# Kernel tuning notes

Measured on AMD Instinct MI355X. Metric: run time of the kernel, lower is better.

Reference implementation:

```python
import jax, jax.numpy as jnp
import numpy as np


def setup_inputs() -> dict:
    key = jax.random.key(0)
    ks = jax.random.split(key, 5)
    B, S, H = 4, 4096, 512
    std = 1.0 / np.sqrt(H)
    x = jax.random.normal(ks[0], (B, S, H), dtype=jnp.float32)
    relative_pos = jax.random.normal(ks[1], (B, S, H), dtype=jnp.float32)
    Wq = jax.random.normal(ks[2], (H, H), dtype=jnp.float32) * std
    Wk = jax.random.normal(ks[3], (H, H), dtype=jnp.float32) * std
    Wv = jax.random.normal(ks[4], (H, H), dtype=jnp.float32) * std
    bq = jnp.zeros((H,), dtype=jnp.float32)
    bk = jnp.zeros((H,), dtype=jnp.float32)
    bv = jnp.zeros((H,), dtype=jnp.float32)
    return {"x": x, "relative_pos": relative_pos, "Wq": Wq, "bq": bq,
            "Wk": Wk, "bk": bk, "Wv": Wv, "bv": bv}


def reference(x, relative_pos, Wq, bq, Wk, bk, Wv, bv):
    H = x.shape[-1]
    scale = jnp.sqrt(jnp.asarray(H, dtype=x.dtype))
    # torch Linear: y = x @ W^T + b
    Q = jnp.einsum('bsh,oh->bso', x, Wq) + bq
    K = jnp.einsum('bsh,oh->bso', x, Wk) + bk
    V = jnp.einsum('bsh,oh->bso', x, Wv) + bv
    Kr = jnp.einsum('bsh,oh->bso', relative_pos, Wk) + bk
    # two score terms, each [B,S,S]
    scores = (jnp.einsum('bqd,bkd->bqk', Q, K) +
              jnp.einsum('bqd,bkd->bqk', Q, Kr)) / scale
    weights = jax.nn.softmax(scores, axis=-1)
    return jnp.einsum('bqk,bkd->bqd', weights, V)
```

## Files before the change

### kernel.cpp

```cpp
#include <hip/hip_runtime.h>
#include <stdint.h>

typedef __attribute__((ext_vector_type(8))) short bf16x8;
typedef __attribute__((ext_vector_type(4))) float f32x4;

#define AS1 __attribute__((address_space(1)))
#define AS3 __attribute__((address_space(3)))

__device__ __forceinline__ void gl2lds16(const void* g, void* l) {
    __builtin_amdgcn_global_load_lds((const AS1 void*)g, (AS3 void*)l, 16, 0, 0);
}

__device__ __forceinline__ unsigned short f2bf(float f) {
    uint32_t u = __builtin_bit_cast(uint32_t, f);
    uint32_t r = (u + 0x7fffu + ((u >> 16) & 1u)) >> 16;
    return (unsigned short)r;
}

constexpr int S = 4096;
constexpr int H = 512;
constexpr size_t OFF_XB  = 0;
constexpr size_t OFF_SB  = 16777216;
constexpr size_t OFF_WQB = 33554432;
constexpr size_t OFF_WKB = 34078720;
constexpr size_t OFF_WVB = 34603008;
constexpr size_t OFF_BQK = 35127296;
constexpr size_t OFF_QB  = 35131392;
constexpr size_t OFF_K2B = OFF_QB  + 16777216;
constexpr size_t OFF_VTB = OFF_K2B + 16777216;
constexpr size_t OFF_PB  = OFF_VTB + 16777216;
constexpr size_t OFF_L   = OFF_PB  + 134217728;

__global__ __launch_bounds__(256) void prep_all(const float* __restrict__ x,
                                                const float* __restrict__ rp,
                                                const float* __restrict__ wq,
                                                const float* __restrict__ wk,
                                                const float* __restrict__ wv,
                                                const float* __restrict__ bq,
                                                const float* __restrict__ bk,
                                                unsigned short* __restrict__ xb,
                                                unsigned short* __restrict__ sb,
                                                unsigned short* __restrict__ wqb,
                                                unsigned short* __restrict__ wkb,
                                                unsigned short* __restrict__ wvb,
                                                float* __restrict__ bqk,
                                                float* __restrict__ lrow) {
    if (blockIdx.x < 8192) {
        const int i = (blockIdx.x * 256 + threadIdx.x) * 4;
        float4 xv = *(const float4*)(x + i);
        float4 rv = *(const float4*)(rp + i);
        uint2 xo, so;
        xo.x = (uint32_t)f2bf(xv.x) | ((uint32_t)f2bf(xv.y) << 16);
        xo.y = (uint32_t)f2bf(xv.z) | ((uint32_t)f2bf(xv.w) << 16);
        so.x = (uint32_t)f2bf(xv.x + rv.x) | ((uint32_t)f2bf(xv.y + rv.y) << 16);
        so.y = (uint32_t)f2bf(xv.z + rv.z) | ((uint32_t)f2bf(xv.w + rv.w) << 16);
        *(uint2*)(xb + i) = xo;
        *(uint2*)(sb + i) = so;
    } else {
        const int t = (blockIdx.x - 8192) * 256 + threadIdx.x;
        const int i = t * 4;
        float4 q = *(const float4*)(wq + i);
        float4 k = *(const float4*)(wk + i);
        float4 v = *(const float4*)(wv + i);
        uint2 o;
        o.x = (uint32_t)f2bf(q.x) | ((uint32_t)f2bf(q.y) << 16);
        o.y = (uint32_t)f2bf(q.z) | ((uint32_t)f2bf(q.w) << 16);
        *(uint2*)(wqb + i) = o;
        o.x = (uint32_t)f2bf(k.x) | ((uint32_t)f2bf(k.y) << 16);
        o.y = (uint32_t)f2bf(k.z) | ((uint32_t)f2bf(k.w) << 16);
        *(uint2*)(wkb + i) = o;
        o.x = (uint32_t)f2bf(v.x) | ((uint32_t)f2bf(v.y) << 16);
        o.y = (uint32_t)f2bf(v.z) | ((uint32_t)f2bf(v.w) << 16);
        *(uint2*)(wvb + i) = o;
        if (t < 128) {
            *(float4*)(bqk + t * 4) = *(const float4*)(bq + t * 4);
        } else if (t < 256) {
            const int u = t - 128;
            float4 b = *(const float4*)(bk + u * 4);
            *(float4*)(bqk + 512 + u * 4) = make_float4(2.f * b.x, 2.f * b.y, 2.f * b.z, 2.f * b.w);
        }
        if (t < 4096) {
            *(float4*)(lrow + t * 4) = make_float4(0.f, 0.f, 0.f, 0.f);
        }
    }
}

template <int MODE, int SWZ, int NP64>
__global__ __launch_bounds__(256, 2)
void gemm_bt(const unsigned short* __restrict__ Abase,
             const unsigned short* __restrict__ Bbase,
             void* __restrict__ Cbase,
             int M, int N, int K,
             long long sAz, long long sBz, long long sCz,
             const float* __restrict__ bias_n, long long sBNz,
             const float* __restrict__ bias_m,
             float scale,
             float* __restrict__ rowdiv, long long sRz)
{
    int bx = blockIdx.x, by = blockIdx.y, bz = blockIdx.z;
    if (SWZ) {
        const int gx = gridDim.x, gy = gridDim.y;
        const int id  = bx + gx * (by + gridDim.y * bz);
        const int xcd = id & 7;
        const int k   = id >> 3;
        const int kg  = k / gx;
        bx = k - kg * gx;
        const int g = xcd + 8 * kg;
        const int gz = g / gy;
        by = g - gz * gy;
        bz = gz;
    }
    const int z = bz;
    const unsigned short* A  = Abase + (size_t)z * (size_t)sAz;
    const unsigned short* Bm = Bbase + (size_t)z * (size_t)sBz;
    const int bn = bx * 128;
    const int bm = by * 128;

    constexpr int STAGE_BYTES = NP64 * 32768;
    constexpr int SMEM_BYTES = (MODE == 1) ? STAGE_BYTES
                             : (STAGE_BYTES > 34816 ? STAGE_BYTES : 34816);
    __shared__ __align__(16) char smem[SMEM_BYTES];
    char* As = smem;
    char* Bs = smem + NP64 * 16384;

    const int tid  = threadIdx.x;
    const int wave = tid >> 6;
    const int lane = tid & 63;
    const int lm   = lane & 15;
    const int quad = lane >> 4;
    const int wm   = (wave >> 1) * 64;
    const int wn   = (wave & 1) * 64;

    const int sr = wave * 8 + (lane >> 3);
    const int ss = ((lane & 7) ^ (lane >> 3)) * 8;

    const int sA0 = (quad ^ (lm & 7)) * 16;

    f32x4 acc[4][4] = {};

    for (int k0 = 0; k0 < K; k0 += 64 * NP64) {
        __syncthreads();
        #pragma unroll
        for (int pp = 0; pp < NP64; pp++) {
            const unsigned short* Ap = A  + (size_t)(bm + sr) * K + k0 + pp * 64 + ss;
            const unsigned short* Bp = Bm + (size_t)(bn + sr) * K + k0 + pp * 64 + ss;
            char* Asp = As + pp * 16384 + wave * 1024;
            char* Bsp = Bs + pp * 16384 + wave * 1024;
            #pragma unroll
            for (int c = 0; c < 4; c++) {
                gl2lds16(Ap + (size_t)(c * 32) * K, Asp + c * 4096);
                gl2lds16(Bp + (size_t)(c * 32) * K, Bsp + c * 4096);
            }
        }
        __syncthreads();

        #pragma unroll
        for (int pp = 0; pp < NP64; pp++) {
            #pragma unroll
            for (int ks = 0; ks < 2; ks++) {
                const int so = ks ? (sA0 ^ 64) : sA0;
                bf16x8 af[4], bfr[4];
                #pragma unroll
                for (int t = 0; t < 4; t++)
                    af[t]  = *(const bf16x8*)(As + pp * 16384 + (wm + t * 16 + lm) * 128 + so);
                #pragma unroll
                for (int t = 0; t < 4; t++)
                    bfr[t] = *(const bf16x8*)(Bs + pp * 16384 + (wn + t * 16 + lm) * 128 + so);
                #pragma unroll
                for (int mt = 0; mt < 4; mt++)
                    #pragma unroll
                    for (int nt = 0; nt < 4; nt++)
                        acc[mt][nt] = __builtin_amdgcn_mfma_f32_16x16x32_bf16(af[mt], bfr[nt], acc[mt][nt], 0, 0, 0);
            }
        }
    }

    if (MODE == 1) {
        float* C = (float*)Cbase + (size_t)z * (size_t)sCz;
        const float* rd = rowdiv + (size_t)z * (size_t)sRz;
        #pragma unroll
        for (int mt = 0; mt < 4; mt++) {
            #pragma unroll
            for (int i = 0; i < 4; i++) {
                const int row = bm + wm + mt * 16 + quad * 4 + i;
                const float inv = 1.0f / rd[row];
                const size_t rb = (size_t)row * (size_t)N;
                #pragma unroll
                for (int nt = 0; nt < 4; nt++) {
                    const int col = bn + wn + nt * 16 + lm;
                    C[rb + col] = acc[mt][nt][i] * inv;
                }
            }
        }
    } else {
        unsigned short* C = (unsigned short*)Cbase + (size_t)z * (size_t)sCz;
        const float* bn_ptr = (MODE == 0 && bias_n) ? bias_n + (size_t)z * (size_t)sBNz : nullptr;
        float* lr = (MODE == 2) ? rowdiv + (size_t)z * (size_t)sRz : nullptr;
        unsigned short* Ct = (unsigned short*)smem;
        __syncthreads();
        #pragma unroll
        for (int mt = 0; mt < 4; mt++) {
            #pragma unroll
            for (int i = 0; i < 4; i++) {
                const int r = wm + mt * 16 + quad * 4 + i;
                if (MODE == 0) {
                    const float badd = bias_m ? bias_m[bm + r] : 0.0f;
                    #pragma unroll
                    for (int nt = 0; nt < 4; nt++) {
                        const int col = bn + wn + nt * 16 + lm;
                        float v = acc[mt][nt][i] * scale + badd;
                        if (bn_ptr) v += bn_ptr[col];
                        Ct[r * 136 + wn + nt * 16 + lm] = f2bf(v);
                    }
                } else {
                    float rsum = 0.f;
                    #pragma unroll
                    for (int nt = 0; nt < 4; nt++) {
                        float p = __expf(acc[mt][nt][i] * scale);
                        rsum += p;
                        Ct[r * 136 + wn + nt * 16 + lm] = f2bf(p);
                    }
                    rsum += __shfl_xor(rsum, 1);
                    rsum += __shfl_xor(rsum, 2);
                    rsum += __shfl_xor(rsum, 4);
                    rsum += __shfl_xor(rsum, 8);
                    if (lm == 0) atomicAdd(lr + bm + r, rsum);
                }
            }
        }
        __syncthreads();
        #pragma unroll
        for (int j = 0; j < 8; j++) {
            const int r   = (tid >> 4) + 16 * j;
            const int c16 = tid & 15;
            uint4 vv = *(const uint4*)(Ct + r * 136 + c16 * 8);
            *(uint4*)(C + (size_t)(bm + r) * (size_t)N + bn + c16 * 8) = vv;
        }
    }
}

extern "C" void kernel_launch(void* const* d_in, const int* in_sizes, int n_in,
                              void* d_out, int out_size, void* d_ws, size_t ws_size,
                              hipStream_t stream) {
    const float* x  = (const float*)d_in[0];
    const float* rp = (const float*)d_in[1];
    const float* Wq = (const float*)d_in[2];
    const float* bq = (const float*)d_in[3];
    const float* Wk = (const float*)d_in[4];
    const float* bk = (const float*)d_in[5];
    const float* Wv = (const float*)d_in[6];
    const float* bv = (const float*)d_in[7];

    char* ws = (char*)d_ws;
    unsigned short* xb  = (unsigned short*)(ws + OFF_XB);
    unsigned short* sb  = (unsigned short*)(ws + OFF_SB);
    unsigned short* wqb = (unsigned short*)(ws + OFF_WQB);
    unsigned short* wkb = (unsigned short*)(ws + OFF_WKB);
    unsigned short* wvb = (unsigned short*)(ws + OFF_WVB);
    float*          bqk = (float*)(ws + OFF_BQK);
    unsigned short* qb  = (unsigned short*)(ws + OFF_QB);
    unsigned short* k2b = (unsigned short*)(ws + OFF_K2B);
    unsigned short* vtb = (unsigned short*)(ws + OFF_VTB);
    unsigned short* pb  = (unsigned short*)(ws + OFF_PB);
    float*          lrow = (float*)(ws + OFF_L);

    prep_all<<<8448, 256, 0, stream>>>(x, rp, Wq, Wk, Wv, bq, bk,
                                       xb, sb, wqb, wkb, wvb, bqk, lrow);

    gemm_bt<0, 1, 1><<<dim3(4, 128, 2), 256, 0, stream>>>(
        xb, wqb, qb, 16384, 512, 512,
        8388608, 262144, 8388608,
        bqk, 512, nullptr, 1.0f, nullptr, 0);
    gemm_bt<0, 0, 1><<<dim3(32, 4, 4), 256, 0, stream>>>(
        wvb, xb, vtb, 512, 4096, 512,
        0, (long long)S * H, (long long)S * H,
        nullptr, 0, bv, 1.0f, nullptr, 0);
    gemm_bt<2, 0, 1><<<dim3(32, 32, 4), 256, 0, stream>>>(
        qb, k2b, pb, 4096, 4096, 512,
        (long long)S * H, (long long)S * H, (long long)S * S,
        nullptr, 0, nullptr, 0.044194173824159216f,
        lrow, 4096);
    gemm_bt<1, 1, 2><<<dim3(4, 32, 4), 256, 0, stream>>>(
        pb, vtb, d_out, 4096, 512, 4096,
        (long long)S * S, (long long)S * H, (long long)S * H,
        nullptr, 0, nullptr, 1.0f, lrow, 4096);
}
```

Baseline: 331.8 us.

## Add dedicated 128x256-tile score kernel with fused exp and row-sum epilogue

Replaces the generic MODE 2 GEMM for the QK^T score stage with a specialized kernel. It uses 512 threads and a 128x256 output tile, so each loaded B tile is reused across more rows and fewer blocks are launched. The kernel keeps the fused exp, row-sum atomic and bf16 store epilogue, writing in two 128-column halves through LDS. The larger tile raises register and LDS use per block, which may reduce occupancy. The MODE 2 path in the generic kernel is removed.

```diff
diff --git a/kernel.cpp b/kernel.cpp
--- a/kernel.cpp
+++ b/kernel.cpp
@@ -133,7 +133,6 @@
 
     const int sr = wave * 8 + (lane >> 3);
     const int ss = ((lane & 7) ^ (lane >> 3)) * 8;
-
     const int sA0 = (quad ^ (lm & 7)) * 16;
 
     f32x4 acc[4][4] = {};
@@ -194,8 +193,7 @@
         }
     } else {
         unsigned short* C = (unsigned short*)Cbase + (size_t)z * (size_t)sCz;
-        const float* bn_ptr = (MODE == 0 && bias_n) ? bias_n + (size_t)z * (size_t)sBNz : nullptr;
-        float* lr = (MODE == 2) ? rowdiv + (size_t)z * (size_t)sRz : nullptr;
+        const float* bn_ptr = bias_n ? bias_n + (size_t)z * (size_t)sBNz : nullptr;
         unsigned short* Ct = (unsigned short*)smem;
         __syncthreads();
         #pragma unroll
@@ -203,22 +201,110 @@
             #pragma unroll
             for (int i = 0; i < 4; i++) {
                 const int r = wm + mt * 16 + quad * 4 + i;
-                if (MODE == 0) {
-                    const float badd = bias_m ? bias_m[bm + r] : 0.0f;
-                    #pragma unroll
-                    for (int nt = 0; nt < 4; nt++) {
-                        const int col = bn + wn + nt * 16 + lm;
-                        float v = acc[mt][nt][i] * scale + badd;
-                        if (bn_ptr) v += bn_ptr[col];
-                        Ct[r * 136 + wn + nt * 16 + lm] = f2bf(v);
-                    }
-                } else {
+                const float badd = bias_m ? bias_m[bm + r] : 0.0f;
+                #pragma unroll
+                for (int nt = 0; nt < 4; nt++) {
+                    const int col = bn + wn + nt * 16 + lm;
+                    float v = acc[mt][nt][i] * scale + badd;
+                    if (bn_ptr) v += bn_ptr[col];
+                    Ct[r * 136 + wn + nt * 16 + lm] = f2bf(v);
+                }
+            }
+        }
+        __syncthreads();
+        #pragma unroll
+        for (int j = 0; j < 8; j++) {
+            const int r   = (tid >> 4) + 16 * j;
+            const int c16 = tid & 15;
+            uint4 vv = *(const uint4*)(Ct + r * 136 + c16 * 8);
+            *(uint4*)(C + (size_t)(bm + r) * (size_t)N + bn + c16 * 8) = vv;
+        }
+    }
+}
+
+__global__ __launch_bounds__(512, 4)
+void score_bt(const unsigned short* __restrict__ Qb,
+              const unsigned short* __restrict__ K2b,
+              unsigned short* __restrict__ Pb,
+              float* __restrict__ lrow)
+{
+    constexpr int N  = 4096;
+    constexpr int Kd = 512;
+    constexpr float scale = 0.044194173824159216f;
+    __shared__ __align__(16) char smem[49152];
+    char* As = smem;
+    char* Bs = smem + 16384;
+
+    const int bx = blockIdx.x, by = blockIdx.y, z = blockIdx.z;
+    const int bn = bx * 256;
+    const int bm = by * 128;
+    const unsigned short* Az = Qb  + (size_t)z * (size_t)N * Kd;
+    const unsigned short* Bz = K2b + (size_t)z * (size_t)N * Kd;
+
+    const int tid  = threadIdx.x;
+    const int wave = tid >> 6;
+    const int lane = tid & 63;
+    const int lm   = lane & 15;
+    const int quad = lane >> 4;
+    const int wm   = (wave >> 2) * 64;
+    const int wn   = (wave & 3) * 64;
+
+    const int sr = wave * 8 + (lane >> 3);
+    const int ss = ((lane & 7) ^ (lane >> 3)) * 8;
+    const int sA0 = (quad ^ (lm & 7)) * 16;
+
+    f32x4 acc[4][4] = {};
+
+    for (int k0 = 0; k0 < Kd; k0 += 64) {
+        __syncthreads();
+        const unsigned short* Ap = Az + (size_t)(bm + sr) * Kd + k0 + ss;
+        const unsigned short* Bp = Bz + (size_t)(bn + sr) * Kd + k0 + ss;
+        char* Asp = As + wave * 1024;
+        char* Bsp = Bs + wave * 1024;
+        gl2lds16(Ap,                   Asp);
+        gl2lds16(Ap + (size_t)64 * Kd, Asp + 8192);
+        #pragma unroll
+        for (int c = 0; c < 4; c++)
+            gl2lds16(Bp + (size_t)(c * 64) * Kd, Bsp + c * 8192);
+        __syncthreads();
+
+        #pragma unroll
+        for (int ks = 0; ks < 2; ks++) {
+            const int so = ks ? (sA0 ^ 64) : sA0;
+            bf16x8 af[4], bfr[4];
+            #pragma unroll
+            for (int t = 0; t < 4; t++)
+                af[t]  = *(const bf16x8*)(As + (wm + t * 16 + lm) * 128 + so);
+            #pragma unroll
+            for (int t = 0; t < 4; t++)
+                bfr[t] = *(const bf16x8*)(Bs + (wn + t * 16 + lm) * 128 + so);
+            #pragma unroll
+            for (int mt = 0; mt < 4; mt++)
+                #pragma unroll
+                for (int nt = 0; nt < 4; nt++)
+                    acc[mt][nt] = __builtin_amdgcn_mfma_f32_16x16x32_bf16(af[mt], bfr[nt], acc[mt][nt], 0, 0, 0);
+        }
+    }
+
+    __syncthreads();
+    unsigned short* Ct = (unsigned short*)smem;
+    float* lr = lrow + (size_t)z * 4096;
+    unsigned short* Cz = Pb + (size_t)z * (size_t)N * N;
+
+    #pragma unroll
+    for (int nh = 0; nh < 2; ++nh) {
+        if ((wn >> 7) == nh) {
+            #pragma unroll
+            for (int mt = 0; mt < 4; mt++) {
+                #pragma unroll
+                for (int i = 0; i < 4; i++) {
+                    const int r = wm + mt * 16 + quad * 4 + i;
                     float rsum = 0.f;
                     #pragma unroll
                     for (int nt = 0; nt < 4; nt++) {
                         float p = __expf(acc[mt][nt][i] * scale);
                         rsum += p;
-                        Ct[r * 136 + wn + nt * 16 + lm] = f2bf(p);
+                        Ct[r * 136 + (wn & 64) + nt * 16 + lm] = f2bf(p);
                     }
                     rsum += __shfl_xor(rsum, 1);
                     rsum += __shfl_xor(rsum, 2);
@@ -230,12 +316,13 @@
         }
         __syncthreads();
         #pragma unroll
-        for (int j = 0; j < 8; j++) {
-            const int r   = (tid >> 4) + 16 * j;
+        for (int j = 0; j < 4; j++) {
+            const int r   = (tid >> 4) + 32 * j;
             const int c16 = tid & 15;
             uint4 vv = *(const uint4*)(Ct + r * 136 + c16 * 8);
-            *(uint4*)(C + (size_t)(bm + r) * (size_t)N + bn + c16 * 8) = vv;
-        }
+            *(uint4*)(Cz + (size_t)(bm + r) * (size_t)N + bn + nh * 128 + c16 * 8) = vv;
+        }
+        if (nh == 0) __syncthreads();
     }
 }
 
@@ -275,11 +362,7 @@
         wvb, xb, vtb, 512, 4096, 512,
         0, (long long)S * H, (long long)S * H,
         nullptr, 0, bv, 1.0f, nullptr, 0);
-    gemm_bt<2, 0, 1><<<dim3(32, 32, 4), 256, 0, stream>>>(
-        qb, k2b, pb, 4096, 4096, 512,
-        (long long)S * H, (long long)S * H, (long long)S * S,
-        nullptr, 0, nullptr, 0.044194173824159216f,
-        lrow, 4096);
+    score_bt<<<dim3(16, 32, 4), 512, 0, stream>>>(qb, k2b, pb, lrow);
     gemm_bt<1, 1, 2><<<dim3(4, 32, 4), 256, 0, stream>>>(
         pb, vtb, d_out, 4096, 512, 4096,
         (long long)S * S, (long long)S * H, (long long)S * H,
```

New measurement: 333.4 us. About the same (+0.5%).
